# Optimization experiments

Measured on AMD Instinct MI355X. Metric: run time of the kernel, lower is better.

The kernel has to match this reference:

```python
import jax, jax.numpy as jnp
import numpy as np

N, E, D = 10000, 320000, 256


def setup_inputs() -> dict:
    key = jax.random.key(0)
    ks = jax.random.split(key, 6)
    return {
        "event_emb": jax.random.normal(ks[0], (N, D), jnp.float32),
        "edge_index": jax.random.randint(ks[1], (2, E), 0, N),
        # GCNConv params (weight [D,D] + bias)
        "W1": jax.random.normal(ks[2], (D, D), jnp.float32) / np.sqrt(D).astype(np.float32),
        "b1": jnp.zeros((D,), jnp.float32),
        # GATConv params (shared lin for src/dst when in==out, heads=1, concat=False)
        "W2": jax.random.normal(ks[3], (D, D), jnp.float32) / np.sqrt(D).astype(np.float32),
        "att_src": jax.random.normal(ks[4], (D,), jnp.float32) / np.sqrt(D).astype(np.float32),
        "att_dst": jax.random.normal(ks[5], (D,), jnp.float32) / np.sqrt(D).astype(np.float32),
        "b2": jnp.zeros((D,), jnp.float32),
    }


def _add_self_loops(src, dst, n):
    loop = jnp.arange(n, dtype=src.dtype)
    return jnp.concatenate([src, loop]), jnp.concatenate([dst, loop])


def _gcn_conv(x, W, b, src, dst, n):
    # PyG GCNConv: D^{-1/2} (A+I) D^{-1/2} X W + b ; self-loops already in src/dst
    xw = x @ W  # [N, D]
    deg = jax.ops.segment_sum(jnp.ones(src.shape[0], x.dtype), dst, num_segments=n)
    dinv = jnp.where(deg > 0, jax.lax.rsqrt(deg), 0.0)
    norm = dinv[src] * dinv[dst]  # [E+N]
    agg = jax.ops.segment_sum(xw[src] * norm[:, None], dst, num_segments=n)
    return agg + b


def _gat_conv(x, W, a_src, a_dst, b, src, dst, n):
    # PyG GATConv heads=1, concat=False, negative_slope=0.2, add_self_loops=True
    xw = x @ W  # [N, D]
    e = jax.nn.leaky_relu((xw @ a_src)[src] + (xw @ a_dst)[dst], 0.2)  # [E+N]
    # softmax over incoming edges of each destination node
    m = jax.ops.segment_max(e, dst, num_segments=n)
    ex = jnp.exp(e - m[dst])
    s = jax.ops.segment_sum(ex, dst, num_segments=n)
    alpha = ex / (s[dst] + 1e-16)
    agg = jax.ops.segment_sum(alpha[:, None] * xw[src], dst, num_segments=n)
    return agg + b


def reference(event_emb, edge_index, W1, b1, W2, att_src, att_dst, b2):
    n = event_emb.shape[0]
    src, dst = _add_self_loops(edge_index[0], edge_index[1], n)
    x = jax.nn.relu(_gcn_conv(event_emb, W1, b1, src, dst, n))
    x = jax.nn.relu(_gat_conv(x, W2, att_src, att_dst, b2, src, dst, n))
    return x
```

## Files before the change

kernel.cpp:

```cpp
#include <hip/hip_runtime.h>
#include <hip/hip_fp16.h>

#define D 256
#define UN 8
#define CAP 64
#define NB 157
#define NBA 160
#define ACAP 48
#define EPB 2000

typedef __attribute__((ext_vector_type(4))) float f32x4;
typedef __attribute__((ext_vector_type(8))) _Float16 f16x8;
typedef __attribute__((ext_vector_type(4))) _Float16 half4v;
typedef __attribute__((ext_vector_type(2))) _Float16 half2v;

__device__ __forceinline__ float leaky(float x) { return x > 0.f ? x : 0.2f * x; }

__global__ __launch_bounds__(256) void prep_binA(const float* __restrict__ W1,
                                                 const float* __restrict__ W2,
                                                 _Float16* __restrict__ W1t,
                                                 _Float16* __restrict__ W2t,
                                                 const int* __restrict__ src,
                                                 const int* __restrict__ dst, int E,
                                                 int2* __restrict__ region,
                                                 unsigned* __restrict__ cntA) {
    __shared__ _Float16 tl[64][66];
    __shared__ unsigned bcnt[NB];
    int bidx = (int)blockIdx.x;
    int tid = (int)threadIdx.x;
    if (bidx < 32) {
        const float* W = (bidx & 16) ? W2 : W1;
        _Float16* Wt = (bidx & 16) ? W2t : W1t;
        int tile = bidx & 15, kt = tile >> 2, ct = tile & 3;
        int rr = tid >> 4, c4 = (tid & 15) << 2;
#pragma unroll
        for (int i = 0; i < 4; i++) {
            int row = rr + (i << 4);
            float4 v = *(const float4*)(W + (size_t)(kt * 64 + row) * 256 + ct * 64 + c4);
            tl[row][c4 + 0] = (_Float16)v.x; tl[row][c4 + 1] = (_Float16)v.y;
            tl[row][c4 + 2] = (_Float16)v.z; tl[row][c4 + 3] = (_Float16)v.w;
        }
        __syncthreads();
#pragma unroll
        for (int i = 0; i < 4; i++) {
            int orow = rr + (i << 4);
            half4v o = {tl[c4 + 0][orow], tl[c4 + 1][orow], tl[c4 + 2][orow],
                        tl[c4 + 3][orow]};
            *(half4v*)(Wt + (size_t)(ct * 64 + orow) * 256 + kt * 64 + c4) = o;
        }
        return;
    }
    int a = bidx - 32;
    for (int j = tid; j < NB; j += 256) bcnt[j] = 0;
    __syncthreads();
    int base = a * EPB;
#pragma unroll
    for (int it = 0; it < 2; it++) {
        int slot = it * 1024 + tid * 4;
        if (slot + 3 < EPB) {
            int e = base + slot;
            int4 s4 = *(const int4*)(src + e);
            int4 d4 = *(const int4*)(dst + e);
            int ss[4] = {s4.x, s4.y, s4.z, s4.w};
            int dd[4] = {d4.x, d4.y, d4.z, d4.w};
#pragma unroll
            for (int j = 0; j < 4; j++) {
                int b = dd[j] >> 6;
                unsigned pos = atomicAdd(&bcnt[b], 1u);
                if (pos < ACAP)
                    region[((size_t)b * NBA + a) * ACAP + pos] = make_int2(ss[j], dd[j]);
            }
        }
    }
    __syncthreads();
    for (int j = tid; j < NB; j += 256)
        cntA[(size_t)j * NBA + a] = bcnt[j] < ACAP ? bcnt[j] : ACAP;
}

template <int DOTS, int AF32>
__device__ __forceinline__ void gemm_body(int t, int bid, _Float16* As, _Float16* Bs,
                                          const void* __restrict__ Ap,
                                          const _Float16* __restrict__ Bt,
                                          _Float16* __restrict__ C,
                                          const float* __restrict__ atS,
                                          const float* __restrict__ atD,
                                          float* __restrict__ asrc, float* __restrict__ adst,
                                          int M) {
    int w = t >> 6, l = t & 63;
    int m0 = bid << 5;
    int ar = t >> 2, ac = t & 3;
    int arow = m0 + ar;
    if (AF32 && arow >= M) arow = M - 1;
    const float* aG32 = (const float*)Ap + (size_t)arow * 256 + (ac << 3);
    const _Float16* aG16 = (const _Float16*)Ap + (size_t)arow * 256 + (ac << 3);
    const _Float16* bG = Bt + (size_t)ar * 256 + (ac << 3);
    int sw = ((ar << 2) + (ac ^ ((ar >> 1) & 3))) << 3;
    float4 a32_0, a32_1;
    uint4 a16;
    if constexpr (AF32) {
        a32_0 = *(const float4*)aG32;
        a32_1 = *(const float4*)(aG32 + 4);
    } else {
        a16 = *(const uint4*)aG16;
    }
    uint4 b_r[8];
#pragma unroll
    for (int j = 0; j < 8; j++) b_r[j] = *(const uint4*)(bG + (size_t)(j << 5) * 256);
    f32x4 acc[16];
#pragma unroll
    for (int ni = 0; ni < 16; ni++) acc[ni] = (f32x4){0.f, 0.f, 0.f, 0.f};
    int c16 = l & 15, g = l >> 4;
    int fb = (c16 << 6) + ((g ^ ((c16 >> 1) & 3)) << 4);
    const char* AsB = (const char*)As + (w << 10) + fb;
    const char* BsB = (const char*)Bs + fb;
#pragma unroll
    for (int k0 = 0; k0 < 256; k0 += 32) {
        __syncthreads();
        if constexpr (AF32) {
            f16x8 ah = {(_Float16)a32_0.x, (_Float16)a32_0.y, (_Float16)a32_0.z,
                        (_Float16)a32_0.w, (_Float16)a32_1.x, (_Float16)a32_1.y,
                        (_Float16)a32_1.z, (_Float16)a32_1.w};
            *(f16x8*)(As + sw) = ah;
        } else {
            *(uint4*)(As + sw) = a16;
        }
#pragma unroll
        for (int j = 0; j < 8; j++) *(uint4*)(Bs + sw + (j << 10)) = b_r[j];
        if (k0 + 32 < 256) {
            if constexpr (AF32) {
                a32_0 = *(const float4*)(aG32 + k0 + 32);
                a32_1 = *(const float4*)(aG32 + k0 + 36);
            } else {
                a16 = *(const uint4*)(aG16 + k0 + 32);
            }
#pragma unroll
            for (int j = 0; j < 8; j++)
                b_r[j] = *(const uint4*)(bG + (size_t)(j << 5) * 256 + k0 + 32);
        }
        __syncthreads();
        f16x8 af = *(const f16x8*)AsB;
#pragma unroll
        for (int ni = 0; ni < 16; ni++) {
            f16x8 bf = *(const f16x8*)(BsB + (ni << 10));
            acc[ni] = __builtin_amdgcn_mfma_f32_16x16x32_f16(af, bf, acc[ni], 0, 0, 0);
        }
    }
    float ps[4] = {0.f, 0.f, 0.f, 0.f}, pd[4] = {0.f, 0.f, 0.f, 0.f};
    if constexpr (DOTS) {
#pragma unroll
        for (int ni = 0; ni < 16; ni++) {
            float sv = atS[(ni << 4) + c16];
            float dv = atD[(ni << 4) + c16];
#pragma unroll
            for (int r = 0; r < 4; r++) {
                ps[r] += acc[ni][r] * sv;
                pd[r] += acc[ni][r] * dv;
            }
        }
    }
#pragma unroll
    for (int r = 0; r < 4; r++) {
        int m = m0 + (w << 4) + (g << 2) + r;
        if (m < M) {
#pragma unroll
            for (int ni = 0; ni < 16; ni++)
                C[(size_t)m * 256 + (ni << 4) + c16] = (_Float16)acc[ni][r];
        }
        if constexpr (DOTS) {
#pragma unroll
            for (int off = 1; off < 16; off <<= 1) {
                ps[r] += __shfl_xor(ps[r], off);
                pd[r] += __shfl_xor(pd[r], off);
            }
            if (c16 == 0 && m < M) {
                asrc[m] = ps[r];
                adst[m] = pd[r];
            }
        }
    }
}

__global__ __launch_bounds__(256, 4) void build_gemm1(const float* __restrict__ emb,
                                                      const _Float16* __restrict__ W1t,
                                                      _Float16* __restrict__ xw1h,
                                                      const int2* __restrict__ region,
                                                      const unsigned* __restrict__ cntA,
                                                      unsigned* __restrict__ cnt,
                                                      int* __restrict__ csr, int M,
                                                      int GBH, int GB) {
    __shared__ __align__(16) _Float16 As2[2][32 * 32];
    __shared__ __align__(16) _Float16 Bs2[2][256 * 32];
    __shared__ unsigned lcnt[64];
    __shared__ unsigned cntAs[NBA];
    int bidx = (int)blockIdx.x;
    int tid = (int)threadIdx.x;
    if (bidx < GBH) {
        int half = tid >> 7;
        int tile = bidx * 2 + half;
        if (tile >= GB) tile = GB - 1;
        gemm_body<0, 1>(tid & 127, tile, As2[half], Bs2[half], emb, W1t, xw1h,
                        nullptr, nullptr, nullptr, nullptr, M);
        return;
    }
    int b = bidx - GBH;
    int nb0 = b << 6;
    if (tid < 64) lcnt[tid] = 0;
    if (tid < NBA) cntAs[tid] = cntA[(size_t)b * NBA + tid];
    __syncthreads();
    int wv = tid >> 6, lane = tid & 63;
    int sub = lane >> 4, li = lane & 15;
    const int2* rb = region + (size_t)b * NBA * ACAP;
    for (int kk = wv << 2; kk < NBA; kk += 16) {
        int k = kk + sub;
        unsigned c = cntAs[k];
        const int2* rp = rb + (size_t)k * ACAP;
        for (int i = li; i < (int)c; i += 16) {
            int2 sd = rp[i];
            unsigned pos = atomicAdd(&lcnt[sd.y - nb0], 1u);
            if (pos < CAP) csr[sd.y * CAP + pos] = sd.x;
        }
    }
    __syncthreads();
    if (tid < 64) {
        int node = nb0 + tid;
        if (node < M) cnt[node] = lcnt[tid];
    }
}

__global__ __launch_bounds__(128, 2) void gemm2_att(const _Float16* __restrict__ x1h,
                                                    const _Float16* __restrict__ W2t,
                                                    _Float16* __restrict__ xw2h,
                                                    const float* __restrict__ atS,
                                                    const float* __restrict__ atD,
                                                    float* __restrict__ asrc,
                                                    float* __restrict__ adst, int M) {
    __shared__ __align__(16) _Float16 As[32 * 32];
    __shared__ __align__(16) _Float16 Bs[256 * 32];
    gemm_body<1, 0>((int)threadIdx.x, (int)blockIdx.x, As, Bs, x1h, W2t, xw2h,
                    atS, atD, asrc, adst, M);
}

__global__ void gcn_agg(const _Float16* __restrict__ xw1h, const int* __restrict__ csr,
                        const unsigned* __restrict__ cnt, const float* __restrict__ b1,
                        _Float16* __restrict__ x1h, int n) {
    int node = (blockIdx.x << 2) + (threadIdx.x >> 6);
    if (node >= n) return;
    int lane = threadIdx.x & 63;
    int fb = ((int)blockIdx.y << 7) + (lane << 1);
    unsigned c = cnt[node];
    int deg = (int)(c < CAP ? c : CAP);
    float dd = rsqrtf((float)c + 1.0f);
    int idxv = node;
    if (lane < deg) idxv = csr[node * CAP + lane];
    float dvv = rsqrtf((float)cnt[idxv] + 1.0f);
    float ax[UN][2];
#pragma unroll
    for (int j = 0; j < UN; j++) { ax[j][0] = ax[j][1] = 0.f; }
    {
        half2v v = *(const half2v*)(xw1h + (size_t)node * D + fb);
        ax[0][0] = (float)v[0] * dd;
        ax[0][1] = (float)v[1] * dd;
    }
    int j = 0;
    for (; j + UN <= deg; j += UN) {
        int s[UN];
        float dv[UN];
#pragma unroll
        for (int jj = 0; jj < UN; jj++) {
            s[jj] = __shfl(idxv, j + jj);
            dv[jj] = __shfl(dvv, j + jj);
        }
#pragma unroll
        for (int jj = 0; jj < UN; jj++) {
            half2v u = *(const half2v*)(xw1h + (size_t)s[jj] * D + fb);
            ax[jj][0] += (float)u[0] * dv[jj];
            ax[jj][1] += (float)u[1] * dv[jj];
        }
    }
    for (; j < deg; j++) {
        int s = __shfl(idxv, j);
        float dv = __shfl(dvv, j);
        half2v u = *(const half2v*)(xw1h + (size_t)s * D + fb);
        ax[0][0] += (float)u[0] * dv;
        ax[0][1] += (float)u[1] * dv;
    }
    float a0 = 0.f, a1 = 0.f;
#pragma unroll
    for (int jj = 0; jj < UN; jj++) { a0 += ax[jj][0]; a1 += ax[jj][1]; }
    float2 bb = *(const float2*)(b1 + fb);
    a0 = a0 * dd + bb.x;
    a1 = a1 * dd + bb.y;
    a0 = a0 > 0.f ? a0 : 0.f;
    a1 = a1 > 0.f ? a1 : 0.f;
    half2v o = {(_Float16)a0, (_Float16)a1};
    *(half2v*)(x1h + (size_t)node * D + fb) = o;
}

__global__ void gat_agg(const _Float16* __restrict__ xw2, const int* __restrict__ csr,
                        const unsigned* __restrict__ cnt, const float* __restrict__ asrc,
                        const float* __restrict__ adst, const float* __restrict__ b2,
                        float* __restrict__ out, int n) {
    int node = (blockIdx.x << 2) + (threadIdx.x >> 6);
    if (node >= n) return;
    int lane = threadIdx.x & 63;
    int fb = ((int)blockIdx.y << 7) + (lane << 1);
    float ad = adst[node];
    unsigned c = cnt[node];
    int deg = (int)(c < CAP ? c : CAP);
    int idxv = node;
    if (lane < deg) idxv = csr[node * CAP + lane];
    float asv = asrc[idxv];
    float sj[UN], aj[UN][2];
#pragma unroll
    for (int j = 0; j < UN; j++) { sj[j] = 0.f; aj[j][0] = aj[j][1] = 0.f; }
    {
        float wgt = __expf(leaky(asrc[node] + ad));
        half2v v = *(const half2v*)(xw2 + (size_t)node * D + fb);
        sj[0] = wgt;
        aj[0][0] = (float)v[0] * wgt;
        aj[0][1] = (float)v[1] * wgt;
    }
    int j = 0;
    for (; j + UN <= deg; j += UN) {
        int s[UN];
        float wgt[UN];
#pragma unroll
        for (int jj = 0; jj < UN; jj++) {
            s[jj] = __shfl(idxv, j + jj);
            wgt[jj] = __expf(leaky(__shfl(asv, j + jj) + ad));
        }
#pragma unroll
        for (int jj = 0; jj < UN; jj++) {
            half2v u = *(const half2v*)(xw2 + (size_t)s[jj] * D + fb);
            sj[jj] += wgt[jj];
            aj[jj][0] += (float)u[0] * wgt[jj];
            aj[jj][1] += (float)u[1] * wgt[jj];
        }
    }
    for (; j < deg; j++) {
        int s = __shfl(idxv, j);
        float wgt = __expf(leaky(__shfl(asv, j) + ad));
        half2v u = *(const half2v*)(xw2 + (size_t)s * D + fb);
        sj[0] += wgt;
        aj[0][0] += (float)u[0] * wgt;
        aj[0][1] += (float)u[1] * wgt;
    }
    float a0 = 0.f, a1 = 0.f, ssum = 0.f;
#pragma unroll
    for (int jj = 0; jj < UN; jj++) { ssum += sj[jj]; a0 += aj[jj][0]; a1 += aj[jj][1]; }
    float inv = 1.0f / (ssum + 1e-16f);
    float2 bb = *(const float2*)(b2 + fb);
    float r0 = a0 * inv + bb.x;
    float r1 = a1 * inv + bb.y;
    r0 = r0 > 0.f ? r0 : 0.f;
    r1 = r1 > 0.f ? r1 : 0.f;
    *(float2*)(out + (size_t)node * D + fb) = make_float2(r0, r1);
}


extern "C" void kernel_launch(void* const* d_in, const int* in_sizes, int n_in,
                              void* d_out, int out_size, void* d_ws, size_t ws_size,
                              hipStream_t stream) {
    const float* emb = (const float*)d_in[0];
    const int*   ei  = (const int*)d_in[1];
    const float* W1  = (const float*)d_in[2];
    const float* b1  = (const float*)d_in[3];
    const float* W2  = (const float*)d_in[4];
    const float* atS = (const float*)d_in[5];
    const float* atD = (const float*)d_in[6];
    const float* b2  = (const float*)d_in[7];

    int n = in_sizes[0] / D;
    int E = in_sizes[1] / 2;
    const int* src = ei;
    const int* dst = ei + E;
    int Mpad = ((n + 31) / 32) * 32;

    char* w = (char*)d_ws;
    auto alloc = [&](size_t bytes) -> char* {
        char* p = w;
        w += (bytes + 255) & ~(size_t)255;
        return p;
    };
    unsigned* cnt    = (unsigned*)alloc((size_t)n * 4);
    float*    asrc   = (float*)alloc((size_t)n * 4);
    float*    adst   = (float*)alloc((size_t)n * 4);
    int*      csr    = (int*)alloc((size_t)n * CAP * 4);
    _Float16* x1h    = (_Float16*)alloc((size_t)Mpad * D * 2);
    _Float16* W1t    = (_Float16*)alloc((size_t)D * D * 2);
    _Float16* W2t    = (_Float16*)alloc((size_t)D * D * 2);
    _Float16* xw1h   = (_Float16*)alloc((size_t)n * D * 2);
    int2*     region = (int2*)alloc((size_t)NB * NBA * ACAP * 8);
    unsigned* cntA   = (unsigned*)alloc((size_t)NB * NBA * 4);
    _Float16* xw2h   = xw1h;

    prep_binA<<<32 + NBA, 256, 0, stream>>>(W1, W2, W1t, W2t, src, dst, E, region, cntA);

    int gb = (n + 31) / 32;
    int gbh = (gb + 1) / 2;
    build_gemm1<<<gbh + NB, 256, 0, stream>>>(emb, W1t, xw1h, region, cntA, cnt, csr, n,
                                              gbh, gb);

    int nb = (n + 3) / 4;
    gcn_agg<<<dim3(nb, 2), 256, 0, stream>>>(xw1h, csr, cnt, b1, x1h, n);

    gemm2_att<<<gb, 128, 0, stream>>>(x1h, W2t, xw2h, atS, atD, asrc, adst, n);

    gat_agg<<<dim3(nb, 2), 256, 0, stream>>>(xw2h, csr, cnt, asrc, adst, b2,
                                             (float*)d_out, n);
}
```

Before: 168.8 us.

## Split wavefront into 4 edge groups with 16-byte feature loads in aggregation

Both aggregation kernels now split each 64-lane wavefront into four 16-lane groups. Each group handles a different neighbor edge, and each lane loads 8 fp16 features at once with a 16-byte load instead of 2. This raises the number of gathers in flight per wavefront and widens each memory access, and per-group partial sums are combined with cross-lane xor shuffles at the end. The cost is extra shuffle reduction work and more registers per lane (32 accumulators), and only one group writes the result. Edge weights are zeroed for lanes past the node degree so padded slots add nothing.

```diff
diff --git a/kernel.cpp b/kernel.cpp
--- a/kernel.cpp
+++ b/kernel.cpp
@@ -2,7 +2,6 @@
 #include <hip/hip_fp16.h>
 
 #define D 256
-#define UN 8
 #define CAP 64
 #define NB 157
 #define NBA 160
@@ -12,7 +11,6 @@
 typedef __attribute__((ext_vector_type(4))) float f32x4;
 typedef __attribute__((ext_vector_type(8))) _Float16 f16x8;
 typedef __attribute__((ext_vector_type(4))) _Float16 half4v;
-typedef __attribute__((ext_vector_type(2))) _Float16 half2v;
 
 __device__ __forceinline__ float leaky(float x) { return x > 0.f ? x : 0.2f * x; }
 
@@ -246,54 +244,66 @@
     int node = (blockIdx.x << 2) + (threadIdx.x >> 6);
     if (node >= n) return;
     int lane = threadIdx.x & 63;
-    int fb = ((int)blockIdx.y << 7) + (lane << 1);
+    int g = lane >> 4, d16 = lane & 15;
+    int fb = ((int)blockIdx.y << 7) + (d16 << 3);
     unsigned c = cnt[node];
     int deg = (int)(c < CAP ? c : CAP);
     float dd = rsqrtf((float)c + 1.0f);
     int idxv = node;
     if (lane < deg) idxv = csr[node * CAP + lane];
-    float dvv = rsqrtf((float)cnt[idxv] + 1.0f);
-    float ax[UN][2];
-#pragma unroll
-    for (int j = 0; j < UN; j++) { ax[j][0] = ax[j][1] = 0.f; }
+    float dvv = lane < deg ? rsqrtf((float)cnt[idxv] + 1.0f) : 0.f;
+    const _Float16* xb = xw1h + fb;
+    float ax[4][8];
+#pragma unroll
+    for (int a = 0; a < 4; a++)
+#pragma unroll
+        for (int q = 0; q < 8; q++) ax[a][q] = 0.f;
     {
-        half2v v = *(const half2v*)(xw1h + (size_t)node * D + fb);
-        ax[0][0] = (float)v[0] * dd;
-        ax[0][1] = (float)v[1] * dd;
-    }
+        f16x8 v = *(const f16x8*)(xb + (size_t)node * D);
+        float ws = g == 0 ? dd : 0.f;
+#pragma unroll
+        for (int q = 0; q < 8; q++) ax[0][q] = (float)v[q] * ws;
+    }
+    int nb4 = (deg + 3) >> 2;
     int j = 0;
-    for (; j + UN <= deg; j += UN) {
-        int s[UN];
-        float dv[UN];
-#pragma unroll
-        for (int jj = 0; jj < UN; jj++) {
-            s[jj] = __shfl(idxv, j + jj);
-            dv[jj] = __shfl(dvv, j + jj);
-        }
-#pragma unroll
-        for (int jj = 0; jj < UN; jj++) {
-            half2v u = *(const half2v*)(xw1h + (size_t)s[jj] * D + fb);
-            ax[jj][0] += (float)u[0] * dv[jj];
-            ax[jj][1] += (float)u[1] * dv[jj];
-        }
-    }
-    for (; j < deg; j++) {
-        int s = __shfl(idxv, j);
-        float dv = __shfl(dvv, j);
-        half2v u = *(const half2v*)(xw1h + (size_t)s * D + fb);
-        ax[0][0] += (float)u[0] * dv;
-        ax[0][1] += (float)u[1] * dv;
-    }
-    float a0 = 0.f, a1 = 0.f;
-#pragma unroll
-    for (int jj = 0; jj < UN; jj++) { a0 += ax[jj][0]; a1 += ax[jj][1]; }
-    float2 bb = *(const float2*)(b1 + fb);
-    a0 = a0 * dd + bb.x;
-    a1 = a1 * dd + bb.y;
-    a0 = a0 > 0.f ? a0 : 0.f;
-    a1 = a1 > 0.f ? a1 : 0.f;
-    half2v o = {(_Float16)a0, (_Float16)a1};
-    *(half2v*)(x1h + (size_t)node * D + fb) = o;
+    for (; j + 4 <= nb4; j += 4) {
+        int s[4];
+        float wv[4];
+#pragma unroll
+        for (int a = 0; a < 4; a++) {
+            int e = ((j + a) << 2) + g;
+            s[a] = __shfl(idxv, e);
+            wv[a] = __shfl(dvv, e);
+        }
+        f16x8 u[4];
+#pragma unroll
+        for (int a = 0; a < 4; a++) u[a] = *(const f16x8*)(xb + (size_t)s[a] * D);
+#pragma unroll
+        for (int a = 0; a < 4; a++)
+#pragma unroll
+            for (int q = 0; q < 8; q++) ax[a][q] += (float)u[a][q] * wv[a];
+    }
+    for (; j < nb4; j++) {
+        int e = (j << 2) + g;
+        int s = __shfl(idxv, e);
+        float wv = __shfl(dvv, e);
+        f16x8 u = *(const f16x8*)(xb + (size_t)s * D);
+#pragma unroll
+        for (int q = 0; q < 8; q++) ax[0][q] += (float)u[q] * wv;
+    }
+    float4 bb0 = *(const float4*)(b1 + fb);
+    float4 bb1 = *(const float4*)(b1 + fb + 4);
+    float bv[8] = {bb0.x, bb0.y, bb0.z, bb0.w, bb1.x, bb1.y, bb1.z, bb1.w};
+    _Float16 o[8];
+#pragma unroll
+    for (int q = 0; q < 8; q++) {
+        float v = (ax[0][q] + ax[1][q]) + (ax[2][q] + ax[3][q]);
+        v += __shfl_xor(v, 16);
+        v += __shfl_xor(v, 32);
+        v = v * dd + bv[q];
+        o[q] = (_Float16)(v > 0.f ? v : 0.f);
+    }
+    if (g == 0) *(f16x8*)(x1h + (size_t)node * D + fb) = *(f16x8*)o;
 }
 
 __global__ void gat_agg(const _Float16* __restrict__ xw2, const int* __restrict__ csr,
@@ -303,58 +313,81 @@
     int node = (blockIdx.x << 2) + (threadIdx.x >> 6);
     if (node >= n) return;
     int lane = threadIdx.x & 63;
-    int fb = ((int)blockIdx.y << 7) + (lane << 1);
+    int g = lane >> 4, d16 = lane & 15;
+    int fb = ((int)blockIdx.y << 7) + (d16 << 3);
     float ad = adst[node];
     unsigned c = cnt[node];
     int deg = (int)(c < CAP ? c : CAP);
     int idxv = node;
     if (lane < deg) idxv = csr[node * CAP + lane];
-    float asv = asrc[idxv];
-    float sj[UN], aj[UN][2];
-#pragma unroll
-    for (int j = 0; j < UN; j++) { sj[j] = 0.f; aj[j][0] = aj[j][1] = 0.f; }
+    float wgtv = lane < deg ? __expf(leaky(asrc[idxv] + ad)) : 0.f;
+    const _Float16* xb = xw2 + fb;
+    float aj[4][8], ss[4];
+#pragma unroll
+    for (int a = 0; a < 4; a++) {
+        ss[a] = 0.f;
+#pragma unroll
+        for (int q = 0; q < 8; q++) aj[a][q] = 0.f;
+    }
     {
-        float wgt = __expf(leaky(asrc[node] + ad));
-        half2v v = *(const half2v*)(xw2 + (size_t)node * D + fb);
-        sj[0] = wgt;
-        aj[0][0] = (float)v[0] * wgt;
-        aj[0][1] = (float)v[1] * wgt;
-    }
+        float ws = g == 0 ? __expf(leaky(asrc[node] + ad)) : 0.f;
+        f16x8 v = *(const f16x8*)(xb + (size_t)node * D);
+        ss[0] = ws;
+#pragma unroll
+        for (int q = 0; q < 8; q++) aj[0][q] = (float)v[q] * ws;
+    }
+    int nb4 = (deg + 3) >> 2;
     int j = 0;
-    for (; j + UN <= deg; j += UN) {
-        int s[UN];
-        float wgt[UN];
-#pragma unroll
-        for (int jj = 0; jj < UN; jj++) {
-            s[jj] = __shfl(idxv, j + jj);
-            wgt[jj] = __expf(leaky(__shfl(asv, j + jj) + ad));
-        }
-#pragma unroll
-        for (int jj = 0; jj < UN; jj++) {
-            half2v u = *(const half2v*)(xw2 + (size_t)s[jj] * D + fb);
-            sj[jj] += wgt[jj];
-            aj[jj][0] += (float)u[0] * wgt[jj];
-            aj[jj][1] += (float)u[1] * wgt[jj];
-        }
-    }
-    for (; j < deg; j++) {
-        int s = __shfl(idxv, j);
-        float wgt = __expf(leaky(__shfl(asv, j) + ad));
-        half2v u = *(const half2v*)(xw2 + (size_t)s * D + fb);
-        sj[0] += wgt;
-        aj[0][0] += (float)u[0] * wgt;
-        aj[0][1] += (float)u[1] * wgt;
-    }
-    float a0 = 0.f, a1 = 0.f, ssum = 0.f;
-#pragma unroll
-    for (int jj = 0; jj < UN; jj++) { ssum += sj[jj]; a0 += aj[jj][0]; a1 += aj[jj][1]; }
+    for (; j + 4 <= nb4; j += 4) {
+        int s[4];
+        float wv[4];
+#pragma unroll
+        for (int a = 0; a < 4; a++) {
+            int e = ((j + a) << 2) + g;
+            s[a] = __shfl(idxv, e);
+            wv[a] = __shfl(wgtv, e);
+        }
+        f16x8 u[4];
+#pragma unroll
+        for (int a = 0; a < 4; a++) u[a] = *(const f16x8*)(xb + (size_t)s[a] * D);
+#pragma unroll
+        for (int a = 0; a < 4; a++) {
+            ss[a] += wv[a];
+#pragma unroll
+            for (int q = 0; q < 8; q++) aj[a][q] += (float)u[a][q] * wv[a];
+        }
+    }
+    for (; j < nb4; j++) {
+        int e = (j << 2) + g;
+        int s = __shfl(idxv, e);
+        float wv = __shfl(wgtv, e);
+        f16x8 u = *(const f16x8*)(xb + (size_t)s * D);
+        ss[0] += wv;
+#pragma unroll
+        for (int q = 0; q < 8; q++) aj[0][q] += (float)u[q] * wv;
+    }
+    float ssum = (ss[0] + ss[1]) + (ss[2] + ss[3]);
+    ssum += __shfl_xor(ssum, 16);
+    ssum += __shfl_xor(ssum, 32);
     float inv = 1.0f / (ssum + 1e-16f);
-    float2 bb = *(const float2*)(b2 + fb);
-    float r0 = a0 * inv + bb.x;
-    float r1 = a1 * inv + bb.y;
-    r0 = r0 > 0.f ? r0 : 0.f;
-    r1 = r1 > 0.f ? r1 : 0.f;
-    *(float2*)(out + (size_t)node * D + fb) = make_float2(r0, r1);
+    float4 bb0 = *(const float4*)(b2 + fb);
+    float4 bb1 = *(const float4*)(b2 + fb + 4);
+    float bv[8] = {bb0.x, bb0.y, bb0.z, bb0.w, bb1.x, bb1.y, bb1.z, bb1.w};
+    float r[8];
+#pragma unroll
+    for (int q = 0; q < 8; q++) {
+        float v = (aj[0][q] + aj[1][q]) + (aj[2][q] + aj[3][q]);
+        v += __shfl_xor(v, 16);
+        v += __shfl_xor(v, 32);
+        v = v * inv + bv[q];
+        r[q] = v > 0.f ? v : 0.f;
+    }
+    if (g == 0) {
+        float4 o0 = {r[0], r[1], r[2], r[3]};
+        float4 o1 = {r[4], r[5], r[6], r[7]};
+        *(float4*)(out + (size_t)node * D + fb) = o0;
+        *(float4*)(out + (size_t)node * D + fb + 4) = o1;
+    }
 }
 
 
```

Measured after the change: 162.9 us, median of 2. -3.5%, faster.
